# Performance work log

Hardware: AMD Instinct MI355X
Metric: run time of the kernel (lower is better)

## Reference

```python
import jax, jax.numpy as jnp
import numpy as np

B, S, D, H = 2, 2048, 1024, 16
HD = D // H  # 64

def _make_freqs():
    # flux-style rotation matrices: [1,1,S,HD//2,2,2]
    theta = 10000.0
    inv = 1.0 / (theta ** (np.arange(0, HD, 2, dtype=np.float32) / HD))  # [HD//2]
    pos = np.arange(S, dtype=np.float32)
    ang = pos[:, None] * inv[None, :]  # [S, HD//2]
    cos, sin = np.cos(ang), np.sin(ang)
    rot = np.stack([np.stack([cos, -sin], -1), np.stack([sin, cos], -1)], -2)  # [S,HD//2,2,2]
    return jnp.asarray(rot[None, None], dtype=jnp.float32)

def setup_inputs() -> dict:
    key = jax.random.key(0)
    ks = jax.random.split(key, 9)
    sc = 1.0 / np.sqrt(D)
    return {
        "x": jax.random.normal(ks[0], (B, S, D), jnp.float32),
        "freqs": _make_freqs(),
        "Wq": jax.random.normal(ks[1], (D, D), jnp.float32) * sc,
        "bq": jax.random.normal(ks[2], (D,), jnp.float32) * 0.01,
        "Wk": jax.random.normal(ks[3], (D, D), jnp.float32) * sc,
        "bk": jax.random.normal(ks[4], (D,), jnp.float32) * 0.01,
        "Wv": jax.random.normal(ks[5], (D, D), jnp.float32) * sc,
        "bv": jax.random.normal(ks[6], (D,), jnp.float32) * 0.01,
        "Wo": jax.random.normal(ks[7], (D, D), jnp.float32) * sc,
        "bo": jax.random.normal(ks[8], (D,), jnp.float32) * 0.01,
    }

def _apply_rope(xq, xk, freqs):
    # xq/xk: [B,H,S,HD]; freqs: [1,1,S,HD//2,2,2]
    def rot(t):
        t_ = t.reshape(*t.shape[:-1], -1, 1, 2)  # [B,H,S,HD//2,1,2]
        out = freqs[..., 0] * t_[..., 0] + freqs[..., 1] * t_[..., 1]  # [B,H,S,HD//2,2]
        return out.reshape(t.shape).astype(t.dtype)
    return rot(xq), rot(xk)

def reference(x, freqs, Wq, bq, Wk, bk, Wv, bv, Wo, bo):
    b, s, _ = x.shape
    # QKV projections (torch Linear: x @ W.T + b)
    q = (x @ Wq.T + bq).reshape(b, s, H, HD).transpose(0, 2, 1, 3)  # [B,H,S,HD]
    k = (x @ Wk.T + bk).reshape(b, s, H, HD).transpose(0, 2, 1, 3)
    v = (x @ Wv.T + bv).reshape(b, s, H, HD).transpose(0, 2, 1, 3)
    q, k = _apply_rope(q, k, freqs)
    # scaled dot product attention, no mask, no dropout
    scale = 1.0 / jnp.sqrt(jnp.asarray(HD, x.dtype))
    scores = jnp.einsum("bhqd,bhkd->bhqk", q, k) * scale
    attn = jax.nn.softmax(scores, axis=-1)
    o = jnp.einsum("bhqk,bhkd->bhqd", attn, v)  # [B,H,S,HD]
    o = o.transpose(0, 2, 1, 3).reshape(b, s, D)
    return o @ Wo.T + bo
```

## Files before the change

kernel.cpp:

```cpp
#include <hip/hip_runtime.h>
#include <cmath>

#define B_ 2
#define S_ 2048
#define D_ 1024
#define H_ 16
#define HD_ 64
#define M_ 4096

typedef __attribute__((ext_vector_type(8))) short short8;
typedef __attribute__((ext_vector_type(4))) short short4v;
typedef __attribute__((ext_vector_type(4))) float f32x4;

__device__ __forceinline__ short f2bf(float x) {
    unsigned u = __builtin_bit_cast(unsigned, x);
    u += 0x7fffu + ((u >> 16) & 1u);
    return (short)(u >> 16);
}

__device__ __forceinline__ void gload_lds16(const short* g, short* l) {
    __builtin_amdgcn_global_load_lds(
        (const __attribute__((address_space(1))) unsigned int*)g,
        (__attribute__((address_space(3))) unsigned int*)l, 16, 0, 0);
}

template<int N> __device__ __forceinline__ void vwait() {
    if constexpr (N == 0) asm volatile("s_waitcnt vmcnt(0)" ::: "memory");
    else if constexpr (N == 2) asm volatile("s_waitcnt vmcnt(2)" ::: "memory");
    else if constexpr (N == 3) asm volatile("s_waitcnt vmcnt(3)" ::: "memory");
    else if constexpr (N == 4) asm volatile("s_waitcnt vmcnt(4)" ::: "memory");
}
__device__ __forceinline__ void bar() { __builtin_amdgcn_s_barrier(); }

__global__ __launch_bounds__(256) void cast_all_kernel(
    const float* __restrict__ x,  const float* __restrict__ Wq,
    const float* __restrict__ Wk, const float* __restrict__ Wv,
    const float* __restrict__ Wo,
    short* __restrict__ xb, short* __restrict__ Wqkvb, short* __restrict__ Wob)
{
    const size_t i = (size_t)blockIdx.x * 256 + threadIdx.x;
    const float* src; short* dst; size_t off;
    if (i < 1048576)      { src = x;  dst = xb;              off = i; }
    else if (i < 1310720) { src = Wq; dst = Wqkvb;           off = i - 1048576; }
    else if (i < 1572864) { src = Wk; dst = Wqkvb + 1048576; off = i - 1310720; }
    else if (i < 1835008) { src = Wv; dst = Wqkvb + 2097152; off = i - 1572864; }
    else                  { src = Wo; dst = Wob;             off = i - 1835008; }
    float4 v = ((const float4*)src)[off];
    short4v o = { f2bf(v.x), f2bf(v.y), f2bf(v.z), f2bf(v.w) };
    ((short4v*)dst)[off] = o;
}

__global__ __launch_bounds__(512) void gemm256(
    const short* __restrict__ A, const short* __restrict__ Bw,
    const float* __restrict__ b0p, const float* __restrict__ b1p, const float* __restrict__ b2p,
    const float* __restrict__ freqs,
    short* __restrict__ out0, short* __restrict__ out1, short* __restrict__ out2)
{
    __shared__ __align__(16) short A0[256*32];
    __shared__ __align__(16) short A1[256*32];
    __shared__ __align__(16) short A2[256*32];
    __shared__ __align__(16) short B0[256*32];
    __shared__ __align__(16) short B1[256*32];
    __shared__ __align__(16) short B2[256*32];
    const int t = threadIdx.x;
    const int w = t >> 6;
    const int lane = t & 63;
    const int qd = lane >> 4, l = lane & 15;
    const int bid = blockIdx.x;
    const int wg  = (bid & 7) * 24 + (bid >> 3);
    const int n0 = (wg % 12) * 256;
    const int m0 = (wg / 12) * 256;
    const int wr = (w >> 2) * 128;
    const int wc = (w & 3) * 64;
    const int srow  = lane >> 2;
    const int sslot = ((lane & 3) ^ ((lane >> 3) & 3)) * 8;
    const int rsw = (l >> 1) & 3;

    f32x4 acc[8][4] = {};

    auto STAGE = [&](int c, short* As, short* Bss) {
        const int k0 = c * 32;
        #pragma unroll
        for (int j = 0; j < 2; ++j) {
            const int r0 = (j*8 + w) * 16;
            gload_lds16(A  + (size_t)(m0 + r0 + srow)*1024 + k0 + sslot, &As[r0*32]);
            gload_lds16(Bw + (size_t)(n0 + r0 + srow)*1024 + k0 + sslot, &Bss[r0*32]);
        }
    };

    auto COMP = [&](const short* As, const short* Bss) {
        short8 af[8], bfr[4];
        #pragma unroll
        for (int rt = 0; rt < 8; ++rt)
            af[rt] = *(const short8*)&As[(wr + rt*16 + l)*32 + ((qd ^ rsw) << 3)];
        #pragma unroll
        for (int ct = 0; ct < 4; ++ct)
            bfr[ct] = *(const short8*)&Bss[(wc + ct*16 + l)*32 + ((qd ^ rsw) << 3)];
        #pragma unroll
        for (int rt = 0; rt < 8; ++rt)
            #pragma unroll
            for (int ct = 0; ct < 4; ++ct)
                acc[rt][ct] = __builtin_amdgcn_mfma_f32_16x16x32_bf16(af[rt], bfr[ct], acc[rt][ct], 0, 0, 0);
    };

    STAGE(0, A0, B0);
    STAGE(1, A1, B1);
    for (int p = 0; p <= 27; p += 3) {
        vwait<4>(); bar();
        STAGE(p + 2, A2, B2);
        COMP(A0, B0);
        vwait<4>(); bar();
        STAGE(p + 3, A0, B0);
        COMP(A1, B1);
        vwait<4>(); bar();
        STAGE(p + 4, A1, B1);
        COMP(A2, B2);
    }
    vwait<4>(); bar();
    COMP(A0, B0);
    vwait<0>(); bar();
    COMP(A1, B1);

    const int sel = n0 >> 10;
    const int nb = n0 & 1023;
    const float* bias = (sel == 0) ? b0p : (sel == 1) ? b1p : b2p;
    if (sel < 2) {
        short* outg = (sel == 0) ? out0 : out1;
        #pragma unroll
        for (int rt = 0; rt < 8; ++rt)
            #pragma unroll
            for (int ct = 0; ct < 4; ++ct) {
                const int d = nb + wc + ct*16 + l;
                const float bsv = bias[d];
                const int h = d >> 6, hd = d & 63;
                #pragma unroll
                for (int r = 0; r < 4; ++r) {
                    const int m = m0 + wr + rt*16 + qd*4 + r;
                    const int bb = m >> 11, s = m & 2047;
                    float val = acc[rt][ct][r] + bsv;
                    float pv = __shfl_xor(val, 1);
                    const float* f = freqs + (size_t)s*128 + (size_t)(hd >> 1)*4;
                    float o = (d & 1) ? (f[2]*pv + f[3]*val) : (f[0]*val + f[1]*pv);
                    outg[((size_t)(bb*16 + h)*2048 + s)*64 + hd] = f2bf(o);
                }
            }
    } else {
        #pragma unroll
        for (int rt = 0; rt < 8; ++rt)
            #pragma unroll
            for (int ct = 0; ct < 4; ++ct) {
                const int d = nb + wc + ct*16 + l;
                const float bsv = bias[d];
                const int h = d >> 6, hd = d & 63;
                const int m0r = m0 + wr + rt*16 + qd*4;
                const int bb = m0r >> 11, s0 = m0r & 2047;
                short4v pk;
                #pragma unroll
                for (int r = 0; r < 4; ++r) pk[r] = f2bf(acc[rt][ct][r] + bsv);
                *(short4v*)&out2[((size_t)(bb*16 + h)*64 + hd)*2048 + s0] = pk;
            }
    }
}

template<int TM, int TN>
__global__ __launch_bounds__(256) void gemm_sa2(
    const short* __restrict__ A, const short* __restrict__ Bw,
    const float* __restrict__ b0p, float* __restrict__ out)
{
    constexpr int RT = TM / 32, CT = TN / 32;
    constexpr int LPC = TM/64 + TN/64;
    __shared__ __align__(16) short A0[TM*32];
    __shared__ __align__(16) short A1[TM*32];
    __shared__ __align__(16) short A2[TM*32];
    __shared__ __align__(16) short B0[TN*32];
    __shared__ __align__(16) short B1[TN*32];
    __shared__ __align__(16) short B2[TN*32];
    const int t = threadIdx.x;
    const int w = t >> 6;
    const int lane = t & 63;
    const int qd = lane >> 4, l = lane & 15;
    const int n0 = blockIdx.x * TN, m0 = blockIdx.y * TM;
    const int wr = (w >> 1) * (TM/2), wc = (w & 1) * (TN/2);
    const int srow  = lane >> 2;
    const int sslot = ((lane & 3) ^ ((lane >> 3) & 3)) * 8;
    const int rsw = (l >> 1) & 3;

    f32x4 acc[RT][CT] = {};

    auto STAGE = [&](int c, short* As, short* Bss) {
        const int k0 = c * 32;
        #pragma unroll
        for (int j = 0; j < TM/64; ++j) {
            const int r0 = (j*4 + w) * 16;
            gload_lds16(A + (size_t)(m0 + r0 + srow)*1024 + k0 + sslot, &As[r0*32]);
        }
        #pragma unroll
        for (int j = 0; j < TN/64; ++j) {
            const int r0 = (j*4 + w) * 16;
            gload_lds16(Bw + (size_t)(n0 + r0 + srow)*1024 + k0 + sslot, &Bss[r0*32]);
        }
    };

    auto COMP = [&](const short* As, const short* Bss) {
        short8 af[RT], bfr[CT];
        #pragma unroll
        for (int rt = 0; rt < RT; ++rt)
            af[rt] = *(const short8*)&As[(wr + rt*16 + l)*32 + ((qd ^ rsw) << 3)];
        #pragma unroll
        for (int ct = 0; ct < CT; ++ct)
            bfr[ct] = *(const short8*)&Bss[(wc + ct*16 + l)*32 + ((qd ^ rsw) << 3)];
        #pragma unroll
        for (int rt = 0; rt < RT; ++rt)
            #pragma unroll
            for (int ct = 0; ct < CT; ++ct)
                acc[rt][ct] = __builtin_amdgcn_mfma_f32_16x16x32_bf16(af[rt], bfr[ct], acc[rt][ct], 0, 0, 0);
    };

    STAGE(0, A0, B0);
    STAGE(1, A1, B1);
    for (int p = 0; p <= 27; p += 3) {
        vwait<LPC>(); bar();
        STAGE(p + 2, A2, B2);
        COMP(A0, B0);
        vwait<LPC>(); bar();
        STAGE(p + 3, A0, B0);
        COMP(A1, B1);
        vwait<LPC>(); bar();
        STAGE(p + 4, A1, B1);
        COMP(A2, B2);
    }
    vwait<LPC>(); bar();
    COMP(A0, B0);
    vwait<0>(); bar();
    COMP(A1, B1);

    #pragma unroll
    for (int rt = 0; rt < RT; ++rt)
        #pragma unroll
        for (int ct = 0; ct < CT; ++ct) {
            const int n = n0 + wc + ct*16 + l;
            const float bias = b0p[n];
            #pragma unroll
            for (int r = 0; r < 4; ++r) {
                const int m = m0 + wr + rt*16 + qd*4 + r;
                out[(size_t)m*1024 + n] = acc[rt][ct][r] + bias;
            }
        }
}

__global__ __launch_bounds__(512) void attn_mfma(
    const short* __restrict__ qg, const short* __restrict__ kg,
    const short* __restrict__ vtg, short* __restrict__ og)
{
    __shared__ __align__(16) short K0[64*64];
    __shared__ __align__(16) short K1[64*64];
    __shared__ __align__(16) short K2[64*64];
    __shared__ __align__(16) short V0[64*64];
    __shared__ __align__(16) short V1[64*64];
    __shared__ __align__(16) short V2[64*64];
    __shared__ __align__(16) short Pb[128*64];

    const int t = threadIdx.x;
    const int w = t >> 6;
    const int lane = t & 63;
    const int qd = lane >> 4, l = lane & 15;
    const int l7 = lane & 7;
    const int q0 = blockIdx.x * 128;
    const int bh = blockIdx.y;

    const int rl  = lane >> 3;
    const int ss8 = ((lane & 7) ^ rl) << 3;

    short8 qf[2];
    const short* qb = qg + ((size_t)bh*2048 + q0 + w*16)*64;
    #pragma unroll
    for (int kf = 0; kf < 2; ++kf)
        qf[kf] = *(const short8*)&qb[l*64 + kf*32 + qd*8];

    f32x4 oacc[4] = {};
    float lsum = 0.f;

    const short* kbase = kg  + (size_t)bh*2048*64;
    const short* vbase = vtg + (size_t)bh*64*2048;
    const float SC = 0.125f * 1.44269504088896340736f;

    auto PREF = [&](int c, short* Kd, short* Vd) {
        gload_lds16(kbase + (size_t)(c*64 + w*8 + rl)*64 + ss8,   &Kd[(w*8)*64]);
        gload_lds16(vbase + (size_t)(w*8 + rl)*2048 + c*64 + ss8, &Vd[(w*8)*64]);
    };

    auto TILE = [&](const short* Kc, const short* Vc) {
        f32x4 sacc[4] = {};
        #pragma unroll
        for (int ct = 0; ct < 4; ++ct) {
            short8 k0f = *(const short8*)&Kc[(ct*16 + l)*64 + (((0 + qd) ^ l7) << 3)];
            short8 k1f = *(const short8*)&Kc[(ct*16 + l)*64 + (((4 + qd) ^ l7) << 3)];
            sacc[ct] = __builtin_amdgcn_mfma_f32_16x16x32_bf16(k0f, qf[0], sacc[ct], 0, 0, 0);
            sacc[ct] = __builtin_amdgcn_mfma_f32_16x16x32_bf16(k1f, qf[1], sacc[ct], 0, 0, 0);
        }
        #pragma unroll
        for (int ct = 0; ct < 4; ++ct) {
            float p0 = exp2f(sacc[ct][0] * SC);
            float p1 = exp2f(sacc[ct][1] * SC);
            float p2 = exp2f(sacc[ct][2] * SC);
            float p3 = exp2f(sacc[ct][3] * SC);
            lsum += (p0 + p1) + (p2 + p3);
            union { unsigned u[2]; short4v s; } cv;
            asm("v_cvt_pk_bf16_f32 %0, %1, %2" : "=v"(cv.u[0]) : "v"(p0), "v"(p1));
            asm("v_cvt_pk_bf16_f32 %0, %1, %2" : "=v"(cv.u[1]) : "v"(p2), "v"(p3));
            *(short4v*)&Pb[(w*16 + l)*64 + (((ct*32 + qd*8) ^ (l7 << 4)) >> 1)] = cv.s;
        }
        #pragma unroll
        for (int kf = 0; kf < 2; ++kf) {
            const int so = ((kf*4 + qd) ^ l7) << 3;
            short8 pa = *(const short8*)&Pb[(w*16 + l)*64 + so];
            #pragma unroll
            for (int ht = 0; ht < 4; ++ht) {
                short8 vb = *(const short8*)&Vc[(ht*16 + l)*64 + so];
                oacc[ht] = __builtin_amdgcn_mfma_f32_16x16x32_bf16(pa, vb, oacc[ht], 0, 0, 0);
            }
        }
    };

    PREF(0, K0, V0);
    PREF(1, K1, V1);
    for (int p = 0; p <= 27; p += 3) {
        vwait<2>(); bar();
        PREF(p + 2, K2, V2);
        TILE(K0, V0);
        vwait<2>(); bar();
        PREF(p + 3, K0, V0);
        TILE(K1, V1);
        vwait<2>(); bar();
        PREF(p + 4, K1, V1);
        TILE(K2, V2);
    }
    vwait<2>(); bar();
    TILE(K0, V0);
    vwait<0>(); bar();
    TILE(K1, V1);

    lsum += __shfl_xor(lsum, 16);
    lsum += __shfl_xor(lsum, 32);
    float inv[4];
    #pragma unroll
    for (int r = 0; r < 4; ++r)
        inv[r] = 1.0f / __shfl(lsum, qd*4 + r);

    const int bb = bh >> 4, h = bh & 15;
    #pragma unroll
    for (int ht = 0; ht < 4; ++ht)
        #pragma unroll
        for (int r = 0; r < 4; ++r) {
            const int s = q0 + w*16 + qd*4 + r;
            og[((size_t)bb*2048 + s)*1024 + h*64 + ht*16 + l] =
                f2bf(oacc[ht][r] * inv[r]);
        }
}

extern "C" void kernel_launch(void* const* d_in, const int* in_sizes, int n_in,
                              void* d_out, int out_size, void* d_ws, size_t ws_size,
                              hipStream_t stream)
{
    const float* x  = (const float*)d_in[0];
    const float* fr = (const float*)d_in[1];
    const float* Wq = (const float*)d_in[2];
    const float* bq = (const float*)d_in[3];
    const float* Wk = (const float*)d_in[4];
    const float* bk = (const float*)d_in[5];
    const float* Wv = (const float*)d_in[6];
    const float* bv = (const float*)d_in[7];
    const float* Wo = (const float*)d_in[8];
    const float* bo = (const float*)d_in[9];
    float* out = (float*)d_out;

    short* ws    = (short*)d_ws;
    short* xb    = ws;
    short* Wqkvb = xb    + 4194304;
    short* Wob   = Wqkvb + 3145728;
    short* qg    = Wob   + 1048576;
    short* kg    = qg    + 4194304;
    short* vtg   = kg    + 4194304;
    short* og    = vtg   + 4194304;

    cast_all_kernel<<<8192, 256, 0, stream>>>(x, Wq, Wk, Wv, Wo, xb, Wqkvb, Wob);
    gemm256<<<192, 512, 0, stream>>>(xb, Wqkvb, bq, bk, bv, fr, qg, kg, vtg);
    attn_mfma<<<dim3(16, 32), 512, 0, stream>>>(qg, kg, vtg, og);
    gemm_sa2<128,64><<<dim3(16, 32), 256, 0, stream>>>(og, Wob, bo, out);
}
```

Before: 246.8 us.

## Retile QKV and output GEMMs and double-pair the attention KV prefetch

The QKV projection moves from 256x256 tiles on 192 blocks of 512 threads to 128x128 tiles on 768 blocks of 256 threads, keeping the fused bias and RoPE epilogue. The output projection becomes a 64x64-tile kernel with a K-step of 64 on 1024 blocks. Attention now prefetches two KV tiles per stage into four buffers and waits for all loads before each pair of tiles. The aim is more blocks per GPU and better occupancy, at the cost of less data reuse per tile and a coarser wait/barrier pattern in attention.

```diff
diff --git a/kernel.cpp b/kernel.cpp
--- a/kernel.cpp
+++ b/kernel.cpp
@@ -50,125 +50,13 @@
     ((short4v*)dst)[off] = o;
 }
 
-__global__ __launch_bounds__(512) void gemm256(
+__global__ __launch_bounds__(256) void gemm_qkv(
     const short* __restrict__ A, const short* __restrict__ Bw,
     const float* __restrict__ b0p, const float* __restrict__ b1p, const float* __restrict__ b2p,
     const float* __restrict__ freqs,
     short* __restrict__ out0, short* __restrict__ out1, short* __restrict__ out2)
 {
-    __shared__ __align__(16) short A0[256*32];
-    __shared__ __align__(16) short A1[256*32];
-    __shared__ __align__(16) short A2[256*32];
-    __shared__ __align__(16) short B0[256*32];
-    __shared__ __align__(16) short B1[256*32];
-    __shared__ __align__(16) short B2[256*32];
-    const int t = threadIdx.x;
-    const int w = t >> 6;
-    const int lane = t & 63;
-    const int qd = lane >> 4, l = lane & 15;
-    const int bid = blockIdx.x;
-    const int wg  = (bid & 7) * 24 + (bid >> 3);
-    const int n0 = (wg % 12) * 256;
-    const int m0 = (wg / 12) * 256;
-    const int wr = (w >> 2) * 128;
-    const int wc = (w & 3) * 64;
-    const int srow  = lane >> 2;
-    const int sslot = ((lane & 3) ^ ((lane >> 3) & 3)) * 8;
-    const int rsw = (l >> 1) & 3;
-
-    f32x4 acc[8][4] = {};
-
-    auto STAGE = [&](int c, short* As, short* Bss) {
-        const int k0 = c * 32;
-        #pragma unroll
-        for (int j = 0; j < 2; ++j) {
-            const int r0 = (j*8 + w) * 16;
-            gload_lds16(A  + (size_t)(m0 + r0 + srow)*1024 + k0 + sslot, &As[r0*32]);
-            gload_lds16(Bw + (size_t)(n0 + r0 + srow)*1024 + k0 + sslot, &Bss[r0*32]);
-        }
-    };
-
-    auto COMP = [&](const short* As, const short* Bss) {
-        short8 af[8], bfr[4];
-        #pragma unroll
-        for (int rt = 0; rt < 8; ++rt)
-            af[rt] = *(const short8*)&As[(wr + rt*16 + l)*32 + ((qd ^ rsw) << 3)];
-        #pragma unroll
-        for (int ct = 0; ct < 4; ++ct)
-            bfr[ct] = *(const short8*)&Bss[(wc + ct*16 + l)*32 + ((qd ^ rsw) << 3)];
-        #pragma unroll
-        for (int rt = 0; rt < 8; ++rt)
-            #pragma unroll
-            for (int ct = 0; ct < 4; ++ct)
-                acc[rt][ct] = __builtin_amdgcn_mfma_f32_16x16x32_bf16(af[rt], bfr[ct], acc[rt][ct], 0, 0, 0);
-    };
-
-    STAGE(0, A0, B0);
-    STAGE(1, A1, B1);
-    for (int p = 0; p <= 27; p += 3) {
-        vwait<4>(); bar();
-        STAGE(p + 2, A2, B2);
-        COMP(A0, B0);
-        vwait<4>(); bar();
-        STAGE(p + 3, A0, B0);
-        COMP(A1, B1);
-        vwait<4>(); bar();
-        STAGE(p + 4, A1, B1);
-        COMP(A2, B2);
-    }
-    vwait<4>(); bar();
-    COMP(A0, B0);
-    vwait<0>(); bar();
-    COMP(A1, B1);
-
-    const int sel = n0 >> 10;
-    const int nb = n0 & 1023;
-    const float* bias = (sel == 0) ? b0p : (sel == 1) ? b1p : b2p;
-    if (sel < 2) {
-        short* outg = (sel == 0) ? out0 : out1;
-        #pragma unroll
-        for (int rt = 0; rt < 8; ++rt)
-            #pragma unroll
-            for (int ct = 0; ct < 4; ++ct) {
-                const int d = nb + wc + ct*16 + l;
-                const float bsv = bias[d];
-                const int h = d >> 6, hd = d & 63;
-                #pragma unroll
-                for (int r = 0; r < 4; ++r) {
-                    const int m = m0 + wr + rt*16 + qd*4 + r;
-                    const int bb = m >> 11, s = m & 2047;
-                    float val = acc[rt][ct][r] + bsv;
-                    float pv = __shfl_xor(val, 1);
-                    const float* f = freqs + (size_t)s*128 + (size_t)(hd >> 1)*4;
-                    float o = (d & 1) ? (f[2]*pv + f[3]*val) : (f[0]*val + f[1]*pv);
-                    outg[((size_t)(bb*16 + h)*2048 + s)*64 + hd] = f2bf(o);
-                }
-            }
-    } else {
-        #pragma unroll
-        for (int rt = 0; rt < 8; ++rt)
-            #pragma unroll
-            for (int ct = 0; ct < 4; ++ct) {
-                const int d = nb + wc + ct*16 + l;
-                const float bsv = bias[d];
-                const int h = d >> 6, hd = d & 63;
-                const int m0r = m0 + wr + rt*16 + qd*4;
-                const int bb = m0r >> 11, s0 = m0r & 2047;
-                short4v pk;
-                #pragma unroll
-                for (int r = 0; r < 4; ++r) pk[r] = f2bf(acc[rt][ct][r] + bsv);
-                *(short4v*)&out2[((size_t)(bb*16 + h)*64 + hd)*2048 + s0] = pk;
-            }
-    }
-}
-
-template<int TM, int TN>
-__global__ __launch_bounds__(256) void gemm_sa2(
-    const short* __restrict__ A, const short* __restrict__ Bw,
-    const float* __restrict__ b0p, float* __restrict__ out)
-{
-    constexpr int RT = TM / 32, CT = TN / 32;
-    constexpr int LPC = TM/64 + TN/64;
+    constexpr int TM = 128, TN = 128, RT = 4, CT = 4, LPC = 4;
     __shared__ __align__(16) short A0[TM*32];
     __shared__ __align__(16) short A1[TM*32];
     __shared__ __align__(16) short A2[TM*32];
@@ -234,10 +122,125 @@
     vwait<0>(); bar();
     COMP(A1, B1);
 
+    const int sel = n0 >> 10;
+    const int nb = n0 & 1023;
+    const float* bias = (sel == 0) ? b0p : (sel == 1) ? b1p : b2p;
+    if (sel < 2) {
+        short* outg = (sel == 0) ? out0 : out1;
+        #pragma unroll
+        for (int rt = 0; rt < RT; ++rt)
+            #pragma unroll
+            for (int ct = 0; ct < CT; ++ct) {
+                const int d = nb + wc + ct*16 + l;
+                const float bsv = bias[d];
+                const int h = d >> 6, hd = d & 63;
+                #pragma unroll
+                for (int r = 0; r < 4; ++r) {
+                    const int m = m0 + wr + rt*16 + qd*4 + r;
+                    const int bb = m >> 11, s = m & 2047;
+                    float val = acc[rt][ct][r] + bsv;
+                    float pv = __shfl_xor(val, 1);
+                    const float* f = freqs + (size_t)s*128 + (size_t)(hd >> 1)*4;
+                    float o = (d & 1) ? (f[2]*pv + f[3]*val) : (f[0]*val + f[1]*pv);
+                    outg[((size_t)(bb*16 + h)*2048 + s)*64 + hd] = f2bf(o);
+                }
+            }
+    } else {
+        #pragma unroll
+        for (int rt = 0; rt < RT; ++rt)
+            #pragma unroll
+            for (int ct = 0; ct < CT; ++ct) {
+                const int d = nb + wc + ct*16 + l;
+                const float bsv = bias[d];
+                const int h = d >> 6, hd = d & 63;
+                const int m0r = m0 + wr + rt*16 + qd*4;
+                const int bb = m0r >> 11, s0 = m0r & 2047;
+                short4v pk;
+                #pragma unroll
+                for (int r = 0; r < 4; ++r) pk[r] = f2bf(acc[rt][ct][r] + bsv);
+                *(short4v*)&out2[((size_t)(bb*16 + h)*64 + hd)*2048 + s0] = pk;
+            }
+    }
+}
+
+__global__ __launch_bounds__(256) void gemm_proj64(
+    const short* __restrict__ A, const short* __restrict__ Bw,
+    const float* __restrict__ b0p, float* __restrict__ out)
+{
+    __shared__ __align__(16) short A0[64*64];
+    __shared__ __align__(16) short A1[64*64];
+    __shared__ __align__(16) short A2[64*64];
+    __shared__ __align__(16) short B0[64*64];
+    __shared__ __align__(16) short B1[64*64];
+    __shared__ __align__(16) short B2[64*64];
+    const int t = threadIdx.x;
+    const int w = t >> 6;
+    const int lane = t & 63;
+    const int qd = lane >> 4, l = lane & 15;
+    const int l7 = lane & 7;
+    const int n0 = blockIdx.x * 64, m0 = blockIdx.y * 64;
+    const int wr = (w >> 1) * 32, wc = (w & 1) * 32;
+    const int rl  = lane >> 3;
+    const int ss8 = ((lane & 7) ^ rl) << 3;
+
+    f32x4 acc[2][2] = {};
+
+    auto STAGE = [&](int c, short* As, short* Bss) {
+        const int k0 = c * 64;
+        #pragma unroll
+        for (int j = 0; j < 2; ++j) {
+            const int r0 = (j*4 + w) * 8;
+            gload_lds16(A  + (size_t)(m0 + r0 + rl)*1024 + k0 + ss8, &As[r0*64]);
+            gload_lds16(Bw + (size_t)(n0 + r0 + rl)*1024 + k0 + ss8, &Bss[r0*64]);
+        }
+    };
+
+    auto COMP = [&](const short* As, const short* Bss) {
+        #pragma unroll
+        for (int kk = 0; kk < 2; ++kk) {
+            short8 af[2], bfr[2];
+            #pragma unroll
+            for (int rt = 0; rt < 2; ++rt)
+                af[rt] = *(const short8*)&As[(wr + rt*16 + l)*64 + (((kk*4 + qd) ^ l7) << 3)];
+            #pragma unroll
+            for (int ct = 0; ct < 2; ++ct)
+                bfr[ct] = *(const short8*)&Bss[(wc + ct*16 + l)*64 + (((kk*4 + qd) ^ l7) << 3)];
+            #pragma unroll
+            for (int rt = 0; rt < 2; ++rt)
+                #pragma unroll
+                for (int ct = 0; ct < 2; ++ct)
+                    acc[rt][ct] = __builtin_amdgcn_mfma_f32_16x16x32_bf16(af[rt], bfr[ct], acc[rt][ct], 0, 0, 0);
+        }
+    };
+
+    STAGE(0, A0, B0);
+    STAGE(1, A1, B1);
+    for (int p = 0; p <= 9; p += 3) {
+        vwait<4>(); bar();
+        STAGE(p + 2, A2, B2);
+        COMP(A0, B0);
+        vwait<4>(); bar();
+        STAGE(p + 3, A0, B0);
+        COMP(A1, B1);
+        vwait<4>(); bar();
+        STAGE(p + 4, A1, B1);
+        COMP(A2, B2);
+    }
+    vwait<4>(); bar();
+    STAGE(14, A2, B2);
+    COMP(A0, B0);
+    vwait<4>(); bar();
+    STAGE(15, A0, B0);
+    COMP(A1, B1);
+    vwait<4>(); bar();
+    COMP(A2, B2);
+    vwait<0>(); bar();
+    COMP(A0, B0);
+
     #pragma unroll
-    for (int rt = 0; rt < RT; ++rt)
-        #pragma unroll
-        for (int ct = 0; ct < CT; ++ct) {
+    for (int rt = 0; rt < 2; ++rt)
+        #pragma unroll
+        for (int ct = 0; ct < 2; ++ct) {
             const int n = n0 + wc + ct*16 + l;
             const float bias = b0p[n];
             #pragma unroll
@@ -252,12 +255,14 @@
     const short* __restrict__ qg, const short* __restrict__ kg,
     const short* __restrict__ vtg, short* __restrict__ og)
 {
-    __shared__ __align__(16) short K0[64*64];
-    __shared__ __align__(16) short K1[64*64];
-    __shared__ __align__(16) short K2[64*64];
-    __shared__ __align__(16) short V0[64*64];
-    __shared__ __align__(16) short V1[64*64];
-    __shared__ __align__(16) short V2[64*64];
+    __shared__ __align__(16) short Ka[64*64];
+    __shared__ __align__(16) short Kb[64*64];
+    __shared__ __align__(16) short Kc[64*64];
+    __shared__ __align__(16) short Kd[64*64];
+    __shared__ __align__(16) short Va[64*64];
+    __shared__ __align__(16) short Vb[64*64];
+    __shared__ __align__(16) short Vc[64*64];
+    __shared__ __align__(16) short Vd[64*64];
     __shared__ __align__(16) short Pb[128*64];
 
     const int t = threadIdx.x;
@@ -284,17 +289,17 @@
     const short* vbase = vtg + (size_t)bh*64*2048;
     const float SC = 0.125f * 1.44269504088896340736f;
 
-    auto PREF = [&](int c, short* Kd, short* Vd) {
-        gload_lds16(kbase + (size_t)(c*64 + w*8 + rl)*64 + ss8,   &Kd[(w*8)*64]);
-        gload_lds16(vbase + (size_t)(w*8 + rl)*2048 + c*64 + ss8, &Vd[(w*8)*64]);
-    };
-
-    auto TILE = [&](const short* Kc, const short* Vc) {
+    auto PREF = [&](int c, short* Kdst, short* Vdst) {
+        gload_lds16(kbase + (size_t)(c*64 + w*8 + rl)*64 + ss8,   &Kdst[(w*8)*64]);
+        gload_lds16(vbase + (size_t)(w*8 + rl)*2048 + c*64 + ss8, &Vdst[(w*8)*64]);
+    };
+
+    auto TILE = [&](const short* Kc_, const short* Vc_) {
         f32x4 sacc[4] = {};
         #pragma unroll
         for (int ct = 0; ct < 4; ++ct) {
-            short8 k0f = *(const short8*)&Kc[(ct*16 + l)*64 + (((0 + qd) ^ l7) << 3)];
-            short8 k1f = *(const short8*)&Kc[(ct*16 + l)*64 + (((4 + qd) ^ l7) << 3)];
+            short8 k0f = *(const short8*)&Kc_[(ct*16 + l)*64 + (((0 + qd) ^ l7) << 3)];
+            short8 k1f = *(const short8*)&Kc_[(ct*16 + l)*64 + (((4 + qd) ^ l7) << 3)];
             sacc[ct] = __builtin_amdgcn_mfma_f32_16x16x32_bf16(k0f, qf[0], sacc[ct], 0, 0, 0);
             sacc[ct] = __builtin_amdgcn_mfma_f32_16x16x32_bf16(k1f, qf[1], sacc[ct], 0, 0, 0);
         }
@@ -316,29 +321,21 @@
             short8 pa = *(const short8*)&Pb[(w*16 + l)*64 + so];
             #pragma unroll
             for (int ht = 0; ht < 4; ++ht) {
-                short8 vb = *(const short8*)&Vc[(ht*16 + l)*64 + so];
+                short8 vb = *(const short8*)&Vc_[(ht*16 + l)*64 + so];
                 oacc[ht] = __builtin_amdgcn_mfma_f32_16x16x32_bf16(pa, vb, oacc[ht], 0, 0, 0);
             }
         }
     };
 
-    PREF(0, K0, V0);
-    PREF(1, K1, V1);
-    for (int p = 0; p <= 27; p += 3) {
-        vwait<2>(); bar();
-        PREF(p + 2, K2, V2);
-        TILE(K0, V0);
-        vwait<2>(); bar();
-        PREF(p + 3, K0, V0);
-        TILE(K1, V1);
-        vwait<2>(); bar();
-        PREF(p + 4, K1, V1);
-        TILE(K2, V2);
+    PREF(0, Ka, Va); PREF(1, Kb, Vb);
+    for (int P = 0; P < 16; P += 2) {
+        vwait<0>(); bar();
+        if (P < 15) { PREF(2*P + 2, Kc, Vc); PREF(2*P + 3, Kd, Vd); }
+        TILE(Ka, Va); TILE(Kb, Vb);
+        vwait<0>(); bar();
+        if (P + 2 < 16) { PREF(2*P + 4, Ka, Va); PREF(2*P + 5, Kb, Vb); }
+        TILE(Kc, Vc); TILE(Kd, Vd);
     }
-    vwait<2>(); bar();
-    TILE(K0, V0);
-    vwait<0>(); bar();
-    TILE(K1, V1);
 
     lsum += __shfl_xor(lsum, 16);
     lsum += __shfl_xor(lsum, 32);
@@ -384,7 +381,7 @@
     short* og    = vtg   + 4194304;
 
     cast_all_kernel<<<8192, 256, 0, stream>>>(x, Wq, Wk, Wv, Wo, xb, Wqkvb, Wob);
-    gemm256<<<192, 512, 0, stream>>>(xb, Wqkvb, bq, bk, bv, fr, qg, kg, vtg);
+    gemm_qkv<<<dim3(24, 32), 256, 0, stream>>>(xb, Wqkvb, bq, bk, bv, fr, qg, kg, vtg);
     attn_mfma<<<dim3(16, 32), 512, 0, stream>>>(qg, kg, vtg, og);
-    gemm_sa2<128,64><<<dim3(16, 32), 256, 0, stream>>>(og, Wob, bo, out);
-}
+    gemm_proj64<<<dim3(16, 64), 256, 0, stream>>>(og, Wob, bo, out);
+}
```

Measured after the change: 254.4 us. 1.03x slower.
